# Kernel optimization log

Measured on AMD Instinct MI355X. Metric: run time of the kernel, lower is better.

Reference implementation:

```python
import jax, jax.numpy as jnp
import numpy as np

NUM_HEADS = 8
NUM_GROUPS = 8
EPS = 1e-5

def group_norm(x, scale, bias):
    b, c, h, w = x.shape
    xg = x.reshape(b, NUM_GROUPS, c // NUM_GROUPS, h, w)
    mean = xg.mean(axis=(2, 3, 4), keepdims=True)
    var = xg.var(axis=(2, 3, 4), keepdims=True)
    xn = ((xg - mean) / jnp.sqrt(var + EPS)).reshape(b, c, h, w)
    return xn * scale[None, :, None, None] + bias[None, :, None, None]

def setup_inputs() -> dict:
    key = jax.random.key(0)
    ks = jax.random.split(key, 7)
    C = 512
    x = jax.random.normal(ks[0], (16, C, 32, 32), dtype=jnp.float32)
    gn_scale = jnp.ones((C,), jnp.float32)
    gn_bias = jnp.zeros((C,), jnp.float32)
    w_qkv = jax.random.normal(ks[1], (3 * C, C), dtype=jnp.float32) * (1.0 / np.sqrt(C))
    b_qkv = jax.random.normal(ks[2], (3 * C,), dtype=jnp.float32) * 0.01
    w_proj = jax.random.normal(ks[3], (C, C), dtype=jnp.float32) * (1.0 / np.sqrt(C))
    b_proj = jax.random.normal(ks[4], (C,), dtype=jnp.float32) * 0.01
    return {"x": x, "gn_scale": gn_scale, "gn_bias": gn_bias,
            "w_qkv": w_qkv, "b_qkv": b_qkv, "w_proj": w_proj, "b_proj": b_proj}

def reference(x, gn_scale, gn_bias, w_qkv, b_qkv, w_proj, b_proj):
    b, c, h, w = x.shape
    hd = c // NUM_HEADS
    hn = group_norm(x, gn_scale, gn_bias)
    # 1x1 conv == per-pixel linear: [b,3c,h,w]
    qkv = jnp.einsum('oc,bchw->bohw', w_qkv, hn) + b_qkv[None, :, None, None]
    q, k, v = jnp.split(qkv, 3, axis=1)
    # -> [b, heads, seq, head_dim], seq = h*w
    def to_heads(t):
        return t.reshape(b, NUM_HEADS, hd, h * w).transpose(0, 1, 3, 2)
    q, k, v = to_heads(q), to_heads(k), to_heads(v)
    scale = 1.0 / jnp.sqrt(jnp.asarray(hd, x.dtype))
    attn = jnp.einsum('bnqd,bnkd->bnqk', q, k) * scale
    attn = jax.nn.softmax(attn, axis=-1)
    out = jnp.einsum('bnqk,bnkd->bnqd', attn, v)
    out = out.transpose(0, 1, 3, 2).reshape(b, c, h, w)
    out = jnp.einsum('oc,bchw->bohw', w_proj, out) + b_proj[None, :, None, None]
    return x + out
```

## Files before the change

kernel.cpp:

```cpp
#include <hip/hip_runtime.h>

typedef _Float16 half8 __attribute__((ext_vector_type(8)));
typedef _Float16 half4 __attribute__((ext_vector_type(4)));
typedef float f32x4 __attribute__((ext_vector_type(4)));

__device__ inline unsigned short f2h(float f) {
  union { _Float16 h; unsigned short u; } cv;
  cv.h = (_Float16)f;
  return cv.u;
}

__device__ inline unsigned int pk2(float a, float b) {
  return __builtin_bit_cast(unsigned int, __builtin_amdgcn_cvt_pkrtz(a, b));
}

__device__ inline void gload_lds16(const void* g, void* l) {
  __builtin_amdgcn_global_load_lds(
      (const __attribute__((address_space(1))) void*)g,
      (__attribute__((address_space(3))) void*)l, 16, 0, 0);
}

__global__ __launch_bounds__(256) void prep(const float* __restrict__ wqkv,
                                            const float* __restrict__ wproj,
                                            _Float16* __restrict__ wq,
                                            _Float16* __restrict__ wp,
                                            const float* __restrict__ x,
                                            float* __restrict__ mr) {
  if (blockIdx.x < 3072) {
    const int i = blockIdx.x * 256 + threadIdx.x;
    wq[i] = (_Float16)wqkv[i];
    if (i < 262144) wp[i] = (_Float16)wproj[i];
    return;
  }
  const int sb = blockIdx.x - 3072;
  const float4* xv = (const float4*)(x + (size_t)sb * 32768);
  float s = 0.f, s2 = 0.f;
  for (int i = threadIdx.x; i < 8192; i += 256) {
    float4 v = xv[i];
    s += v.x + v.y + v.z + v.w;
    s2 += v.x * v.x + v.y * v.y + v.z * v.z + v.w * v.w;
  }
  for (int m = 32; m; m >>= 1) {
    s += __shfl_down(s, m);
    s2 += __shfl_down(s2, m);
  }
  __shared__ float ls[4], ls2[4];
  const int wid = threadIdx.x >> 6;
  if ((threadIdx.x & 63) == 0) { ls[wid] = s; ls2[wid] = s2; }
  __syncthreads();
  if (threadIdx.x == 0) {
    mr[sb * 2] = ls[0] + ls[1] + ls[2] + ls[3];
    mr[sb * 2 + 1] = ls2[0] + ls2[1] + ls2[2] + ls2[3];
  }
}

__global__ __launch_bounds__(256) void gn_apply(const float* __restrict__ x,
                                                const float* __restrict__ mr,
                                                const float* __restrict__ sc,
                                                const float* __restrict__ bi,
                                                _Float16* __restrict__ hn) {
  __shared__ __align__(16) _Float16 t[64][72];
  const int b = blockIdx.z, cb = blockIdx.y, pb = blockIdx.x;
  const int c0 = cb * 64, p0 = pb * 64;
  const int bg = b * 8 + cb;
  const float S = mr[bg * 4 + 0] + mr[bg * 4 + 2];
  const float S2 = mr[bg * 4 + 1] + mr[bg * 4 + 3];
  const float mean = S * (1.f / 65536.f);
  const float var = S2 * (1.f / 65536.f) - mean * mean;
  const float rstd = rsqrtf(var + 1e-5f);
  const int tp = threadIdx.x & 63;
  const int tc = threadIdx.x >> 6;
#pragma unroll
  for (int i = 0; i < 16; i++) {
    const int c = tc * 16 + i;
    const float g = sc[c0 + c] * rstd;
    const float v = x[((size_t)b * 512 + c0 + c) * 1024 + p0 + tp];
    t[tp][c] = (_Float16)((v - mean) * g + bi[c0 + c]);
  }
  __syncthreads();
  const int wp = threadIdx.x >> 2;
  const int wc = (threadIdx.x & 3) * 16;
  _Float16* dst = hn + ((size_t)b * 1024 + p0 + wp) * 512 + c0 + wc;
  *(uint4*)dst = *(const uint4*)&t[wp][wc];
  *(uint4*)(dst + 8) = *(const uint4*)&t[wp][wc + 8];
}

template <int EPI>
__global__ __launch_bounds__(512, 4) void gemm_mfma(
    const _Float16* __restrict__ A, const _Float16* __restrict__ Bt,
    const float* __restrict__ bias, const float* __restrict__ xin,
    float* __restrict__ fout, _Float16* __restrict__ qo,
    _Float16* __restrict__ ko, _Float16* __restrict__ vo) {
  __shared__ __align__(16) _Float16 As[128 * 64];
  __shared__ __align__(16) _Float16 Bs[128 * 64];
  const int b = blockIdx.z;
  const int m0 = blockIdx.y * 128, n0 = blockIdx.x * 128;
  const char* Ab = (const char*)A;
  const char* Bb = (const char*)(Bt + (size_t)b * 1024 * 512);
  const int t = threadIdx.x, lane = t & 63, w = t >> 6;
  const int wm = (w & 1) * 64, wn = (w >> 1) * 32;
  const int lr = lane & 15, lk = lane >> 4;
  int srow[2], scb[2];
#pragma unroll
  for (int it = 0; it < 2; it++) {
    srow[it] = it * 64 + (t >> 3);
    scb[it] = ((t & 7) * 16) ^ ((srow[it] & 7) << 4);
  }
  f32x4 acc[4][2] = {};
#pragma unroll 1
  for (int k0 = 0; k0 < 512; k0 += 64) {
#pragma unroll
    for (int it = 0; it < 2; it++) {
      const size_t go = (size_t)(m0 + srow[it]) * 1024 + k0 * 2 + scb[it];
      const size_t gob = (size_t)(n0 + srow[it]) * 1024 + k0 * 2 + scb[it];
      char* la = (char*)As + it * 8192 + w * 1024 + (lane & 63) * 16;
      char* lb = (char*)Bs + it * 8192 + w * 1024 + (lane & 63) * 16;
      gload_lds16(Ab + go, la - (lane & 63) * 16);
      gload_lds16(Bb + gob, lb - (lane & 63) * 16);
    }
    __syncthreads();
#pragma unroll
    for (int kk = 0; kk < 2; kk++) {
      half8 af[4], bf[2];
#pragma unroll
      for (int i = 0; i < 4; i++) {
        const int ra = wm + i * 16 + lr;
        af[i] = *(const half8*)((const char*)As +
                                ((ra * 128 + kk * 64 + lk * 16) ^ ((ra & 7) << 4)));
      }
#pragma unroll
      for (int j = 0; j < 2; j++) {
        const int rb = wn + j * 16 + lr;
        bf[j] = *(const half8*)((const char*)Bs +
                                ((rb * 128 + kk * 64 + lk * 16) ^ ((rb & 7) << 4)));
      }
#pragma unroll
      for (int i = 0; i < 4; i++)
#pragma unroll
        for (int j = 0; j < 2; j++)
          acc[i][j] = __builtin_amdgcn_mfma_f32_16x16x32_f16(af[i], bf[j],
                                                             acc[i][j], 0, 0, 0);
    }
    __syncthreads();
  }
#pragma unroll
  for (int i = 0; i < 4; i++) {
    const int o = m0 + wm + i * 16 + lk * 4;
#pragma unroll
    for (int j = 0; j < 2; j++) {
      const int p = n0 + wn + j * 16 + lr;
      float vv[4];
#pragma unroll
      for (int r = 0; r < 4; r++) vv[r] = acc[i][j][r] + bias[o + r];
      if (EPI == 0) {
        const int sec = o >> 9, oc = o & 511;
        const int h = oc >> 6, d0 = oc & 63;
        if (sec == 0) {
          const float qs = 0.125f * 1.44269504f;
          ushort4 pk;
          pk.x = f2h(vv[0] * qs); pk.y = f2h(vv[1] * qs);
          pk.z = f2h(vv[2] * qs); pk.w = f2h(vv[3] * qs);
          *(ushort4*)(qo + ((size_t)(b * 8 + h) * 1024 + p) * 64 + d0) = pk;
        } else if (sec == 1) {
          ushort4 pk;
          pk.x = f2h(vv[0]); pk.y = f2h(vv[1]);
          pk.z = f2h(vv[2]); pk.w = f2h(vv[3]);
          *(ushort4*)(ko + ((size_t)(b * 8 + h) * 1024 + p) * 64 + d0) = pk;
        } else {
#pragma unroll
          for (int r = 0; r < 4; r++)
            vo[((size_t)(b * 8 + h) * 64 + d0 + r) * 1024 + p] = (_Float16)vv[r];
        }
      } else {
        const size_t idx = ((size_t)b * 512 + o) * 1024 + p;
#pragma unroll
        for (int r = 0; r < 4; r++)
          fout[idx + (size_t)r * 1024] = xin[idx + (size_t)r * 1024] + vv[r];
      }
    }
  }
}

__global__ __launch_bounds__(512, 4) void attn(const _Float16* __restrict__ q,
                                               const _Float16* __restrict__ k,
                                               const _Float16* __restrict__ v,
                                               _Float16* __restrict__ o) {
  __shared__ __align__(16) _Float16 KT[2][4096];
  __shared__ __align__(16) _Float16 VT[2][4096];
  __shared__ __align__(16) _Float16 PT[8][2048];
  const int id = blockIdx.x;
  const int flat = (id & 7) * 64 + (id >> 3);
  const int qb = flat & 3, bh = flat >> 2;
  const int b = bh >> 3, h = bh & 7;
  const int t = threadIdx.x, lane = t & 63, w = t >> 6;
  const int lr = lane & 15, lk = lane >> 4;
  const int q0 = qb * 256 + w * 32;
  const _Float16* qp = q + (size_t)bh * 65536;
  const char* kc = (const char*)(k + (size_t)bh * 65536);
  const char* vc = (const char*)(v + (size_t)bh * 65536);
  const int srow = t >> 3, scol = (t & 7) * 16;
  const int sdst = srow * 128 + (scol ^ ((srow & 7) << 4));
  int koff[4][2];
#pragma unroll
  for (int j = 0; j < 4; j++) {
    const int row = j * 16 + lr, sw = (row & 7) << 4;
    koff[j][0] = row * 128 + ((lk * 16) ^ sw);
    koff[j][1] = row * 128 + ((64 + lk * 16) ^ sw);
  }
  int pwoff[2][4];
#pragma unroll
  for (int g = 0; g < 2; g++) {
    const int qhat = g * 16 + lr, sw = (qhat & 7) << 4;
#pragma unroll
    for (int j = 0; j < 4; j++)
      pwoff[g][j] = qhat * 128 + ((j * 32 + lk * 8) ^ sw);
  }
  half8 qf[2][2];
#pragma unroll
  for (int g = 0; g < 2; g++)
#pragma unroll
    for (int kk = 0; kk < 2; kk++)
      qf[g][kk] = *(const half8*)(qp + (q0 + g * 16 + lr) * 64 + kk * 32 + lk * 8);
  const half8 onesv = {(_Float16)1.f, (_Float16)1.f, (_Float16)1.f, (_Float16)1.f,
                       (_Float16)1.f, (_Float16)1.f, (_Float16)1.f, (_Float16)1.f};
  {
    uint4 k0 = *(const uint4*)(kc + srow * 128 + scol);
    uint4 v0 = *(const uint4*)(vc + srow * 2048 + scol);
    *(uint4*)((char*)KT + sdst) = k0;
    *(uint4*)((char*)VT + sdst) = v0;
  }
  __syncthreads();
  f32x4 aco[2][4] = {};
  f32x4 lacc[2] = {};
  char* Pc = (char*)PT + w * 4096;
#pragma unroll 1
  for (int kt = 0; kt < 16; kt++) {
    const int cur = kt & 1;
    const char* Kc = (const char*)KT + cur * 8192;
    const char* Vc = (const char*)VT + cur * 8192;
    uint4 kn, vn;
    if (kt < 15) {
      kn = *(const uint4*)(kc + (kt + 1) * 8192 + srow * 128 + scol);
      vn = *(const uint4*)(vc + srow * 2048 + (kt + 1) * 128 + scol);
    }
    f32x4 s[2][4];
#pragma unroll
    for (int g = 0; g < 2; g++)
#pragma unroll
      for (int j = 0; j < 4; j++) {
        s[g][j][0] = -10.f; s[g][j][1] = -10.f;
        s[g][j][2] = -10.f; s[g][j][3] = -10.f;
      }
    __builtin_amdgcn_s_setprio(1);
#pragma unroll
    for (int j = 0; j < 4; j++) {
      const half8 kf0 = *(const half8*)(Kc + koff[j][0]);
      const half8 kf1 = *(const half8*)(Kc + koff[j][1]);
#pragma unroll
      for (int g = 0; g < 2; g++) {
        s[g][j] = __builtin_amdgcn_mfma_f32_16x16x32_f16(kf0, qf[g][0], s[g][j], 0, 0, 0);
        s[g][j] = __builtin_amdgcn_mfma_f32_16x16x32_f16(kf1, qf[g][1], s[g][j], 0, 0, 0);
      }
    }
    __builtin_amdgcn_s_setprio(0);
#pragma unroll
    for (int g = 0; g < 2; g++) {
#pragma unroll
      for (int j = 0; j < 4; j++) {
        uint2 pw;
        pw.x = pk2(__builtin_amdgcn_exp2f(s[g][j][0]),
                   __builtin_amdgcn_exp2f(s[g][j][1]));
        pw.y = pk2(__builtin_amdgcn_exp2f(s[g][j][2]),
                   __builtin_amdgcn_exp2f(s[g][j][3]));
        *(uint2*)(Pc + pwoff[g][j]) = pw;
      }
    }
    __builtin_amdgcn_s_setprio(1);
#pragma unroll
    for (int kk = 0; kk < 2; kk++) {
      half8 vf[4];
#pragma unroll
      for (int jd = 0; jd < 4; jd++)
        vf[jd] = *(const half8*)(Vc + koff[jd][kk]);
#pragma unroll
      for (int g = 0; g < 2; g++) {
        const half8 pf = *(const half8*)(Pc + koff[g][kk]);
        lacc[g] = __builtin_amdgcn_mfma_f32_16x16x32_f16(pf, onesv, lacc[g], 0, 0, 0);
#pragma unroll
        for (int jd = 0; jd < 4; jd++)
          aco[g][jd] = __builtin_amdgcn_mfma_f32_16x16x32_f16(pf, vf[jd], aco[g][jd], 0, 0, 0);
      }
    }
    __builtin_amdgcn_s_setprio(0);
    if (kt < 15) {
      *(uint4*)((char*)KT + (cur ^ 1) * 8192 + sdst) = kn;
      *(uint4*)((char*)VT + (cur ^ 1) * 8192 + sdst) = vn;
    }
    __syncthreads();
  }
#pragma unroll
  for (int g = 0; g < 2; g++)
#pragma unroll
    for (int r = 0; r < 4; r++) {
      const float rl = 1.f / lacc[g][r];
      const int row = q0 + g * 16 + 4 * lk + r;
#pragma unroll
      for (int jd = 0; jd < 4; jd++)
        o[((size_t)b * 1024 + row) * 512 + h * 64 + jd * 16 + lr] =
            (_Float16)(aco[g][jd][r] * rl);
    }
}

extern "C" void kernel_launch(void* const* d_in, const int* in_sizes, int n_in,
                              void* d_out, int out_size, void* d_ws, size_t ws_size,
                              hipStream_t stream) {
  const float* x = (const float*)d_in[0];
  const float* gsc = (const float*)d_in[1];
  const float* gbi = (const float*)d_in[2];
  const float* wqkv = (const float*)d_in[3];
  const float* bqkv = (const float*)d_in[4];
  const float* wproj = (const float*)d_in[5];
  const float* bproj = (const float*)d_in[6];
  float* out = (float*)d_out;
  char* ws = (char*)d_ws;
  float* mr = (float*)ws;
  _Float16* wq16 = (_Float16*)(ws + 4096);
  _Float16* wp16 = (_Float16*)(ws + 4096 + 1572864);
  _Float16* hn = (_Float16*)(ws + 2101248);
  _Float16* q16 = (_Float16*)(ws + 18878464);
  _Float16* k16 = (_Float16*)(ws + 35655680);
  _Float16* v16 = (_Float16*)(ws + 52432896);

  hipLaunchKernelGGL(prep, dim3(3328), dim3(256), 0, stream, wqkv, wproj, wq16,
                     wp16, x, mr);
  hipLaunchKernelGGL(gn_apply, dim3(16, 8, 16), dim3(256), 0, stream, x, mr, gsc,
                     gbi, hn);
  hipLaunchKernelGGL((gemm_mfma<0>), dim3(8, 12, 16), dim3(512), 0, stream, wq16,
                     hn, bqkv, (const float*)nullptr, (float*)nullptr, q16, k16,
                     v16);
  hipLaunchKernelGGL(attn, dim3(512), dim3(512), 0, stream, q16, k16, v16, hn);
  hipLaunchKernelGGL((gemm_mfma<1>), dim3(8, 4, 16), dim3(512), 0, stream, wp16,
                     hn, bproj, x, out, (_Float16*)nullptr, (_Float16*)nullptr,
                     (_Float16*)nullptr);
}
```

Before: 129.0 us.

## Prefetch next GEMM k-tile into registers while computing current tile

Replaces the direct global-to-LDS async loads in the MFMA GEMM with register-staged loads. The next k-tile's global load is issued before the current tile's MFMAs, then written to LDS after a barrier. The aim is to hide global memory latency behind compute, which the old load-then-sync-then-compute loop exposed. It costs extra VGPRs for the staging buffers and an LDS write step, which could pressure occupancy under launch_bounds(512,4).

```diff
diff --git a/kernel.cpp b/kernel.cpp
--- a/kernel.cpp
+++ b/kernel.cpp
@@ -12,12 +12,6 @@
 
 __device__ inline unsigned int pk2(float a, float b) {
   return __builtin_bit_cast(unsigned int, __builtin_amdgcn_cvt_pkrtz(a, b));
-}
-
-__device__ inline void gload_lds16(const void* g, void* l) {
-  __builtin_amdgcn_global_load_lds(
-      (const __attribute__((address_space(1))) void*)g,
-      (__attribute__((address_space(3))) void*)l, 16, 0, 0);
 }
 
 __global__ __launch_bounds__(256) void prep(const float* __restrict__ wqkv,
@@ -100,25 +94,41 @@
   const int t = threadIdx.x, lane = t & 63, w = t >> 6;
   const int wm = (w & 1) * 64, wn = (w >> 1) * 32;
   const int lr = lane & 15, lk = lane >> 4;
-  int srow[2], scb[2];
+  int srow[2], scol[2], sdst[2];
 #pragma unroll
   for (int it = 0; it < 2; it++) {
-    srow[it] = it * 64 + (t >> 3);
-    scb[it] = ((t & 7) * 16) ^ ((srow[it] & 7) << 4);
+    const int flat = it * 512 + t;
+    srow[it] = flat >> 3;
+    scol[it] = (flat & 7) * 16;
+    sdst[it] = srow[it] * 128 + (scol[it] ^ ((srow[it] & 7) << 4));
   }
   f32x4 acc[4][2] = {};
+  {
+    uint4 a0[2], b0[2];
+#pragma unroll
+    for (int it = 0; it < 2; it++) {
+      a0[it] = *(const uint4*)(Ab + (size_t)(m0 + srow[it]) * 1024 + scol[it]);
+      b0[it] = *(const uint4*)(Bb + (size_t)(n0 + srow[it]) * 1024 + scol[it]);
+    }
+#pragma unroll
+    for (int it = 0; it < 2; it++) {
+      *(uint4*)((char*)As + sdst[it]) = a0[it];
+      *(uint4*)((char*)Bs + sdst[it]) = b0[it];
+    }
+  }
+  __syncthreads();
 #pragma unroll 1
   for (int k0 = 0; k0 < 512; k0 += 64) {
-#pragma unroll
-    for (int it = 0; it < 2; it++) {
-      const size_t go = (size_t)(m0 + srow[it]) * 1024 + k0 * 2 + scb[it];
-      const size_t gob = (size_t)(n0 + srow[it]) * 1024 + k0 * 2 + scb[it];
-      char* la = (char*)As + it * 8192 + w * 1024 + (lane & 63) * 16;
-      char* lb = (char*)Bs + it * 8192 + w * 1024 + (lane & 63) * 16;
-      gload_lds16(Ab + go, la - (lane & 63) * 16);
-      gload_lds16(Bb + gob, lb - (lane & 63) * 16);
-    }
-    __syncthreads();
+    uint4 an[2], bn[2];
+    if (k0 < 448) {
+#pragma unroll
+      for (int it = 0; it < 2; it++) {
+        an[it] = *(const uint4*)(Ab + (size_t)(m0 + srow[it]) * 1024 +
+                                 (k0 + 64) * 2 + scol[it]);
+        bn[it] = *(const uint4*)(Bb + (size_t)(n0 + srow[it]) * 1024 +
+                                 (k0 + 64) * 2 + scol[it]);
+      }
+    }
 #pragma unroll
     for (int kk = 0; kk < 2; kk++) {
       half8 af[4], bf[2];
@@ -140,6 +150,14 @@
         for (int j = 0; j < 2; j++)
           acc[i][j] = __builtin_amdgcn_mfma_f32_16x16x32_f16(af[i], bf[j],
                                                              acc[i][j], 0, 0, 0);
+    }
+    __syncthreads();
+    if (k0 < 448) {
+#pragma unroll
+      for (int it = 0; it < 2; it++) {
+        *(uint4*)((char*)As + sdst[it]) = an[it];
+        *(uint4*)((char*)Bs + sdst[it]) = bn[it];
+      }
     }
     __syncthreads();
   }
```

Result: slower. 218.2 us (+69.1%).
